# Kernel tuning notes

Hardware: AMD Instinct MI355X
Metric: run time of the kernel (lower is better)

The kernel has to match this reference:

```python
import math
import jax, jax.numpy as jnp
import numpy as np

SQRT_2_OVER_PI = 0.7978845608028654
FACIL_RATE = 2.0
FIRE_THRESH = 0.88
EPS = 1e-05

def _gelu(x):
    return 0.5 * x * (1.0 + jnp.tanh(SQRT_2_OVER_PI * (x + 0.044715 * x ** 3)))

def setup_inputs() -> dict:
    key = jax.random.key(0)
    ks = jax.random.split(key, 8)
    B, T, D, N = 4, 4096, 1024, 512
    x = jax.random.normal(ks[0], (B, T, D), jnp.float32)
    ema_x = jax.random.normal(ks[1], (D,), jnp.float32) * 0.1
    ema_x2 = ema_x ** 2 + jax.random.uniform(ks[2], (D,), jnp.float32) + 0.5
    ema_y = jax.random.normal(ks[3], (D,), jnp.float32) * 0.1
    ema_y2 = ema_y ** 2 + jax.random.uniform(ks[4], (D,), jnp.float32) + 0.5
    buf = jax.random.normal(ks[5], (N, D), jnp.float32)
    buf = buf / jnp.linalg.norm(buf, axis=-1, keepdims=True)
    facil = 1.0 + 2.0 * jax.random.uniform(ks[6], (N,), jnp.float32)  # facilitation levels >= 1
    mask = jnp.ones((N,), dtype=bool)
    return {
        'x': x,
        'log_tau_in': jnp.float32(math.log(1.0)),
        'log_tau_out': jnp.float32(math.log(1.0)),
        'log_a_in': jnp.float32(0.0),
        'log_a_out': jnp.float32(0.0),
        'log_k_boost': jnp.float32(math.log(0.5)),
        'log_k_damp': jnp.float32(math.log(0.3)),
        'ema_x': ema_x, 'ema_x2': ema_x2, 'ema_y': ema_y, 'ema_y2': ema_y2,
        'buf': buf, 'facil': facil, 'mask': mask,
    }

def reference(x, log_tau_in, log_tau_out, log_a_in, log_a_out,
              log_k_boost, log_k_damp, ema_x, ema_x2, ema_y, ema_y2,
              buf, facil, mask):
    sg = jax.lax.stop_gradient
    D = x.shape[-1]
    y = _gelu(x)
    # --- gate_211 (l1_ready steady state); z-statistics are detached in torch ---
    tau_in, tau_out = jnp.exp(log_tau_in), jnp.exp(log_tau_out)
    a_in, a_out = jax.nn.sigmoid(log_a_in), jax.nn.sigmoid(log_a_out)
    std_x = jnp.sqrt(jnp.clip(sg(ema_x2) - sg(ema_x) ** 2, 0.0)) + EPS
    z_in = jnp.mean(((sg(x) - sg(ema_x)) / std_x) ** 2, axis=-1)        # [B,T]
    std_y = jnp.sqrt(jnp.clip(sg(ema_y2) - sg(ema_y) ** 2, 0.0)) + EPS
    z_out = jnp.mean(((sg(y) - sg(ema_y)) / std_y) ** 2, axis=-1)       # [B,T]
    g_in = 1.0 - a_in + a_in * jnp.exp(-tau_in * z_in)
    g_out = 1.0 - a_out + a_out * jnp.exp(-tau_out * z_out)
    gate = g_in * g_out
    y1 = y * gate[..., None]
    # --- eval-time OCS nearest-neighbor facilitation (l2_ready, pass1_complete) ---
    k_boost = jnp.clip(jnp.exp(log_k_boost), 0.01, 4.0)
    k_damp = jnp.clip(jnp.exp(log_k_damp), 0.01, 0.9)
    y1_mean = jnp.mean(sg(y1).reshape(-1, D), axis=0)                    # [D]
    m_n = y1_mean / jnp.maximum(jnp.linalg.norm(y1_mean), 1e-12)
    buf_sg = sg(buf)
    buf_n = buf_sg / jnp.maximum(jnp.linalg.norm(buf_sg, axis=-1, keepdims=True), 1e-12)
    sims = jnp.where(mask, buf_n @ m_n, -1.0)                            # [N]
    nearest_idx = jnp.argmax(sims)
    sim_val = jnp.clip(sims[nearest_idx], 0.0, 1.0)
    fired = sim_val > FIRE_THRESH
    facil_level = sg(facil)[nearest_idx] * jnp.where(fired, FACIL_RATE, 1.0)
    v = buf_sg[nearest_idx]                                              # [D]
    valid = jnp.all(jnp.isfinite(v)) & (jnp.linalg.norm(v) >= 1e-06)
    mod = (facil_level - 1.0) * sim_val
    boost = 1.0 + sg(k_boost) * mod            # torch uses .item(): detached
    damp = jnp.maximum(0.01, 1.0 - sg(k_damp) * mod)
    proj = jnp.sum(y1 * v, axis=-1, keepdims=True)
    y_par = proj * v
    out = jnp.where(valid, y_par * boost + (y1 - y_par) * damp, y1)
    return out
```

## Files before the change

kernel.cpp:

```cpp
#include <hip/hip_runtime.h>
#include <math.h>

#define D 1024
#define NROWS 16384
#define NBUF 512
#define NBLK_A 512

#define OFF_INVSTDX 0
#define OFF_INVSTDY 1024
#define OFF_CONST   2048
#define OFF_KEY     2056
#define OFF_RES     2058
#define OFF_GATE    2064
#define OFF_MEAN    18448
#define OFF_PART    19472

__device__ __forceinline__ float4 ld4(const float* p) { return *(const float4*)p; }

__device__ __forceinline__ float wave_red(float v) {
    #pragma unroll
    for (int off = 32; off > 0; off >>= 1) v += __shfl_xor(v, off, 64);
    return v;
}

__device__ __forceinline__ float gelu_f(float x) {
    float u = 0.7978845608028654f * (x + 0.044715f * x * x * x);
    float e = __expf(2.0f * u);
    float t = 1.0f - 2.0f / (e + 1.0f);
    return 0.5f * x * (1.0f + t);
}

__global__ void k_init(const float* __restrict__ ema_x, const float* __restrict__ ema_x2,
                       const float* __restrict__ ema_y, const float* __restrict__ ema_y2,
                       const float* __restrict__ lti, const float* __restrict__ lto,
                       const float* __restrict__ lai, const float* __restrict__ lao,
                       float* __restrict__ ws) {
    int t = threadIdx.x;
    if (t < D) {
        float vx = ema_x2[t] - ema_x[t] * ema_x[t]; vx = vx > 0.f ? vx : 0.f;
        ws[OFF_INVSTDX + t] = 1.0f / (sqrtf(vx) + 1e-5f);
        float vy = ema_y2[t] - ema_y[t] * ema_y[t]; vy = vy > 0.f ? vy : 0.f;
        ws[OFF_INVSTDY + t] = 1.0f / (sqrtf(vy) + 1e-5f);
    }
    if (t == 0) {
        ws[OFF_CONST + 0] = expf(lti[0]);
        ws[OFF_CONST + 1] = expf(lto[0]);
        ws[OFF_CONST + 2] = 1.0f / (1.0f + expf(-lai[0]));
        ws[OFF_CONST + 3] = 1.0f / (1.0f + expf(-lao[0]));
        *(unsigned long long*)&ws[OFF_KEY] = 0ull;
    }
}

__global__ __launch_bounds__(256) void k_passA(const float* __restrict__ x,
                                               const float* __restrict__ ema_x,
                                               const float* __restrict__ ema_y,
                                               float* __restrict__ ws) {
    __shared__ float s_acc[D];
    const int tid = threadIdx.x;
    const int wave = tid >> 6, lane = tid & 63;
    for (int i = tid; i < D; i += 256) s_acc[i] = 0.0f;
    __syncthreads();

    const float tau_in = ws[OFF_CONST + 0], tau_out = ws[OFF_CONST + 1];
    const float a_in  = ws[OFF_CONST + 2], a_out  = ws[OFF_CONST + 3];

    int col[4];
    float4 emx[4], isx[4], emy[4], isy[4];
    #pragma unroll
    for (int j = 0; j < 4; ++j) {
        col[j] = 4 * lane + 256 * j;
        emx[j] = ld4(&ema_x[col[j]]);
        isx[j] = ld4(&ws[OFF_INVSTDX + col[j]]);
        emy[j] = ld4(&ema_y[col[j]]);
        isy[j] = ld4(&ws[OFF_INVSTDY + col[j]]);
    }
    float4 acc[4];
    #pragma unroll
    for (int j = 0; j < 4; ++j) acc[j] = make_float4(0.f, 0.f, 0.f, 0.f);

    const int gw = blockIdx.x * 4 + wave;
    const int r0 = gw * 8;
    for (int r = r0; r < r0 + 8; ++r) {
        const float* xr = x + (size_t)r * D;
        float4 yv[4];
        float zin = 0.f, zout = 0.f;
        #pragma unroll
        for (int j = 0; j < 4; ++j) {
            float4 xv = ld4(&xr[col[j]]);
            float dx, dy;
            dx = (xv.x - emx[j].x) * isx[j].x; zin += dx * dx;
            dx = (xv.y - emx[j].y) * isx[j].y; zin += dx * dx;
            dx = (xv.z - emx[j].z) * isx[j].z; zin += dx * dx;
            dx = (xv.w - emx[j].w) * isx[j].w; zin += dx * dx;
            yv[j].x = gelu_f(xv.x); dy = (yv[j].x - emy[j].x) * isy[j].x; zout += dy * dy;
            yv[j].y = gelu_f(xv.y); dy = (yv[j].y - emy[j].y) * isy[j].y; zout += dy * dy;
            yv[j].z = gelu_f(xv.z); dy = (yv[j].z - emy[j].z) * isy[j].z; zout += dy * dy;
            yv[j].w = gelu_f(xv.w); dy = (yv[j].w - emy[j].w) * isy[j].w; zout += dy * dy;
        }
        zin  = wave_red(zin)  * (1.0f / D);
        zout = wave_red(zout) * (1.0f / D);
        float g = ((1.0f - a_in)  + a_in  * __expf(-tau_in  * zin)) *
                  ((1.0f - a_out) + a_out * __expf(-tau_out * zout));
        if (lane == 0) ws[OFF_GATE + r] = g;
        #pragma unroll
        for (int j = 0; j < 4; ++j) {
            acc[j].x += yv[j].x * g;
            acc[j].y += yv[j].y * g;
            acc[j].z += yv[j].z * g;
            acc[j].w += yv[j].w * g;
        }
    }
    #pragma unroll
    for (int j = 0; j < 4; ++j) {
        atomicAdd(&s_acc[col[j] + 0], acc[j].x);
        atomicAdd(&s_acc[col[j] + 1], acc[j].y);
        atomicAdd(&s_acc[col[j] + 2], acc[j].z);
        atomicAdd(&s_acc[col[j] + 3], acc[j].w);
    }
    __syncthreads();
    float4 pv = *(float4*)&s_acc[tid * 4];
    *(float4*)&ws[OFF_PART + (size_t)blockIdx.x * D + tid * 4] = pv;
}

__global__ void k_mean(float* __restrict__ ws) {
    int d = blockIdx.x * 128 + threadIdx.x;
    float s = 0.f;
    const float* p = &ws[OFF_PART];
    for (int b = 0; b < NBLK_A; ++b) s += p[(size_t)b * D + d];
    ws[OFF_MEAN + d] = s * (1.0f / (float)NROWS);
}

__global__ __launch_bounds__(256) void k_sims(const float* __restrict__ buf,
                                              const unsigned char* __restrict__ mask,
                                              float* __restrict__ ws) {
    __shared__ float s_red[4];
    __shared__ float s_inv;
    const int tid = threadIdx.x, wave = tid >> 6, lane = tid & 63;

    float4 mv = ld4(&ws[OFF_MEAN + tid * 4]);
    float ns = mv.x * mv.x + mv.y * mv.y + mv.z * mv.z + mv.w * mv.w;
    ns = wave_red(ns);
    if (lane == 0) s_red[wave] = ns;
    __syncthreads();
    if (tid == 0) {
        float t = s_red[0] + s_red[1] + s_red[2] + s_red[3];
        s_inv = 1.0f / fmaxf(sqrtf(t), 1e-12f);
    }
    __syncthreads();
    const float inv = s_inv;

    int col[4];
    float4 mvv[4];
    #pragma unroll
    for (int j = 0; j < 4; ++j) {
        col[j] = 4 * lane + 256 * j;
        mvv[j] = ld4(&ws[OFF_MEAN + col[j]]);
    }
    unsigned long long* keyp = (unsigned long long*)&ws[OFF_KEY];
    const int gw = blockIdx.x * 4 + wave;
    for (int n = gw * 8; n < gw * 8 + 8; ++n) {
        const float* br = buf + (size_t)n * D;
        float dot = 0.f, bns = 0.f;
        #pragma unroll
        for (int j = 0; j < 4; ++j) {
            float4 bv = ld4(&br[col[j]]);
            dot += bv.x * mvv[j].x + bv.y * mvv[j].y + bv.z * mvv[j].z + bv.w * mvv[j].w;
            bns += bv.x * bv.x + bv.y * bv.y + bv.z * bv.z + bv.w * bv.w;
        }
        dot = wave_red(dot);
        bns = wave_red(bns);
        if (lane == 0) {
            float sim = -1.0f;
            if (mask[n]) sim = (dot * inv) / fmaxf(sqrtf(bns), 1e-12f);
            unsigned int fb = __float_as_uint(sim);
            unsigned int mono = (fb & 0x80000000u) ? ~fb : (fb | 0x80000000u);
            unsigned long long key = ((unsigned long long)mono << 32) | (unsigned int)(~n);
            atomicMax(keyp, key);
        }
    }
}

__global__ __launch_bounds__(1024) void k_final(const float* __restrict__ buf,
                                                const float* __restrict__ facil,
                                                const float* __restrict__ lkb,
                                                const float* __restrict__ lkd,
                                                float* __restrict__ ws) {
    __shared__ float s_sum[16];
    __shared__ int s_fin;
    const int tid = threadIdx.x, wave = tid >> 6, lane = tid & 63;
    if (tid == 0) s_fin = 1;
    __syncthreads();

    unsigned long long key = *(const unsigned long long*)&ws[OFF_KEY];
    int idx = (int)(~(unsigned int)(key & 0xFFFFFFFFull));
    unsigned int mono = (unsigned int)(key >> 32);
    unsigned int fb = (mono & 0x80000000u) ? (mono ^ 0x80000000u) : ~mono;
    float sim = __uint_as_float(fb);

    float v = buf[(size_t)idx * D + tid];
    if (!isfinite(v)) atomicAnd(&s_fin, 0);
    float ns = wave_red(v * v);
    if (lane == 0) s_sum[wave] = ns;
    __syncthreads();
    if (tid == 0) {
        float t = 0.f;
        #pragma unroll
        for (int i = 0; i < 16; ++i) t += s_sum[i];
        float nrm = sqrtf(t);
        int valid = s_fin && (nrm >= 1e-6f);
        float sim_val = fminf(fmaxf(sim, 0.0f), 1.0f);
        float fl = facil[idx] * ((sim_val > 0.88f) ? 2.0f : 1.0f);
        float mod = (fl - 1.0f) * sim_val;
        float kb = fminf(fmaxf(expf(lkb[0]), 0.01f), 4.0f);
        float kd = fminf(fmaxf(expf(lkd[0]), 0.01f), 0.9f);
        float boost = 1.0f + kb * mod;
        float damp = fmaxf(0.01f, 1.0f - kd * mod);
        int* wi = (int*)ws;
        wi[OFF_RES + 0] = idx;
        wi[OFF_RES + 1] = valid;
        ws[OFF_RES + 2] = boost;
        ws[OFF_RES + 3] = damp;
    }
}

__global__ __launch_bounds__(256) void k_passB(const float* __restrict__ x,
                                               const float* __restrict__ buf,
                                               const float* __restrict__ ws,
                                               float* __restrict__ out) {
    const int tid = threadIdx.x, wave = tid >> 6, lane = tid & 63;
    const int* wi = (const int*)ws;
    const int idx = wi[OFF_RES + 0];
    const int valid = wi[OFF_RES + 1];
    const float boost = ws[OFF_RES + 2], damp = ws[OFF_RES + 3];
    const float dampe = valid ? damp : 1.0f;
    const float coef = valid ? (boost - damp) : 0.0f;

    int col[4];
    float4 vv[4];
    const float* vrow = buf + (size_t)idx * D;
    #pragma unroll
    for (int j = 0; j < 4; ++j) {
        col[j] = 4 * lane + 256 * j;
        vv[j] = ld4(&vrow[col[j]]);
        if (!valid) vv[j] = make_float4(0.f, 0.f, 0.f, 0.f);
    }

    const int gw = blockIdx.x * 4 + wave;
    const int r0 = gw * 8;
    for (int r = r0; r < r0 + 8; ++r) {
        const float* xr = x + (size_t)r * D;
        const float g = ws[OFF_GATE + r];
        float4 y1[4];
        float proj = 0.f;
        #pragma unroll
        for (int j = 0; j < 4; ++j) {
            float4 xv = ld4(&xr[col[j]]);
            y1[j].x = gelu_f(xv.x) * g; proj += y1[j].x * vv[j].x;
            y1[j].y = gelu_f(xv.y) * g; proj += y1[j].y * vv[j].y;
            y1[j].z = gelu_f(xv.z) * g; proj += y1[j].z * vv[j].z;
            y1[j].w = gelu_f(xv.w) * g; proj += y1[j].w * vv[j].w;
        }
        proj = wave_red(proj);
        const float pc = proj * coef;
        float* orow = out + (size_t)r * D;
        #pragma unroll
        for (int j = 0; j < 4; ++j) {
            float4 o;
            o.x = y1[j].x * dampe + pc * vv[j].x;
            o.y = y1[j].y * dampe + pc * vv[j].y;
            o.z = y1[j].z * dampe + pc * vv[j].z;
            o.w = y1[j].w * dampe + pc * vv[j].w;
            *(float4*)&orow[col[j]] = o;
        }
    }
}

extern "C" void kernel_launch(void* const* d_in, const int* in_sizes, int n_in,
                              void* d_out, int out_size, void* d_ws, size_t ws_size,
                              hipStream_t stream) {
    const float* x      = (const float*)d_in[0];
    const float* lti    = (const float*)d_in[1];
    const float* lto    = (const float*)d_in[2];
    const float* lai    = (const float*)d_in[3];
    const float* lao    = (const float*)d_in[4];
    const float* lkb    = (const float*)d_in[5];
    const float* lkd    = (const float*)d_in[6];
    const float* ema_x  = (const float*)d_in[7];
    const float* ema_x2 = (const float*)d_in[8];
    const float* ema_y  = (const float*)d_in[9];
    const float* ema_y2 = (const float*)d_in[10];
    const float* buf    = (const float*)d_in[11];
    const float* facil  = (const float*)d_in[12];
    const unsigned char* mask = (const unsigned char*)d_in[13];
    float* ws  = (float*)d_ws;
    float* out = (float*)d_out;

    hipLaunchKernelGGL(k_init,  dim3(1),   dim3(1024), 0, stream,
                       ema_x, ema_x2, ema_y, ema_y2, lti, lto, lai, lao, ws);
    hipLaunchKernelGGL(k_passA, dim3(NBLK_A), dim3(256), 0, stream, x, ema_x, ema_y, ws);
    hipLaunchKernelGGL(k_mean,  dim3(8),   dim3(128),  0, stream, ws);
    hipLaunchKernelGGL(k_sims,  dim3(16),  dim3(256),  0, stream, buf, mask, ws);
    hipLaunchKernelGGL(k_final, dim3(1),   dim3(1024), 0, stream, buf, facil, lkb, lkd, ws);
    hipLaunchKernelGGL(k_passB, dim3(NBLK_A), dim3(256), 0, stream, x, buf, ws, out);
}
```

Before: 213.3 us.

## Fold init and mean kernels into passA, double grid, use nontemporal stores

Removes the separate init and mean-reduction kernels. passA now computes the inverse stds and gate constants inline and adds its per-block column sums directly into the global mean with atomics; a memset clears the workspace first. passA, sims and passB launch twice as many blocks, each handling half as many rows, with occupancy hints. The output is written with nontemporal stores. The mean is left as an unnormalized sum, which is fine because it is only used as a normalized direction, but the global float atomics add contention and make the summation order nondeterministic.

```diff
diff --git a/kernel.cpp b/kernel.cpp
--- a/kernel.cpp
+++ b/kernel.cpp
@@ -4,18 +4,20 @@
 #define D 1024
 #define NROWS 16384
 #define NBUF 512
-#define NBLK_A 512
-
-#define OFF_INVSTDX 0
-#define OFF_INVSTDY 1024
-#define OFF_CONST   2048
-#define OFF_KEY     2056
-#define OFF_RES     2058
-#define OFF_GATE    2064
-#define OFF_MEAN    18448
-#define OFF_PART    19472
+
+#define OFF_MEAN 0
+#define OFF_KEY  1024
+#define OFF_RES  1026
+#define OFF_GATE 1032
+#define ZERO_BYTES 4112
+
+typedef float nfloat4 __attribute__((ext_vector_type(4)));
 
 __device__ __forceinline__ float4 ld4(const float* p) { return *(const float4*)p; }
+__device__ __forceinline__ void st4_nt(float* p, float4 v) {
+    nfloat4 nv = { v.x, v.y, v.z, v.w };
+    __builtin_nontemporal_store(nv, (nfloat4*)p);
+}
 
 __device__ __forceinline__ float wave_red(float v) {
     #pragma unroll
@@ -30,39 +32,34 @@
     return 0.5f * x * (1.0f + t);
 }
 
-__global__ void k_init(const float* __restrict__ ema_x, const float* __restrict__ ema_x2,
-                       const float* __restrict__ ema_y, const float* __restrict__ ema_y2,
-                       const float* __restrict__ lti, const float* __restrict__ lto,
-                       const float* __restrict__ lai, const float* __restrict__ lao,
-                       float* __restrict__ ws) {
-    int t = threadIdx.x;
-    if (t < D) {
-        float vx = ema_x2[t] - ema_x[t] * ema_x[t]; vx = vx > 0.f ? vx : 0.f;
-        ws[OFF_INVSTDX + t] = 1.0f / (sqrtf(vx) + 1e-5f);
-        float vy = ema_y2[t] - ema_y[t] * ema_y[t]; vy = vy > 0.f ? vy : 0.f;
-        ws[OFF_INVSTDY + t] = 1.0f / (sqrtf(vy) + 1e-5f);
-    }
-    if (t == 0) {
-        ws[OFF_CONST + 0] = expf(lti[0]);
-        ws[OFF_CONST + 1] = expf(lto[0]);
-        ws[OFF_CONST + 2] = 1.0f / (1.0f + expf(-lai[0]));
-        ws[OFF_CONST + 3] = 1.0f / (1.0f + expf(-lao[0]));
-        *(unsigned long long*)&ws[OFF_KEY] = 0ull;
-    }
-}
-
-__global__ __launch_bounds__(256) void k_passA(const float* __restrict__ x,
-                                               const float* __restrict__ ema_x,
-                                               const float* __restrict__ ema_y,
-                                               float* __restrict__ ws) {
+__device__ __forceinline__ float4 inv_std4(float4 m, float4 m2) {
+    float4 r;
+    r.x = 1.0f / (sqrtf(fmaxf(m2.x - m.x * m.x, 0.f)) + 1e-5f);
+    r.y = 1.0f / (sqrtf(fmaxf(m2.y - m.y * m.y, 0.f)) + 1e-5f);
+    r.z = 1.0f / (sqrtf(fmaxf(m2.z - m.z * m.z, 0.f)) + 1e-5f);
+    r.w = 1.0f / (sqrtf(fmaxf(m2.w - m.w * m.w, 0.f)) + 1e-5f);
+    return r;
+}
+
+__global__ __launch_bounds__(256, 4) void k_passA(const float* __restrict__ x,
+                                                  const float* __restrict__ ema_x,
+                                                  const float* __restrict__ ema_x2,
+                                                  const float* __restrict__ ema_y,
+                                                  const float* __restrict__ ema_y2,
+                                                  const float* __restrict__ lti,
+                                                  const float* __restrict__ lto,
+                                                  const float* __restrict__ lai,
+                                                  const float* __restrict__ lao,
+                                                  float* __restrict__ ws) {
     __shared__ float s_acc[D];
     const int tid = threadIdx.x;
     const int wave = tid >> 6, lane = tid & 63;
     for (int i = tid; i < D; i += 256) s_acc[i] = 0.0f;
     __syncthreads();
 
-    const float tau_in = ws[OFF_CONST + 0], tau_out = ws[OFF_CONST + 1];
-    const float a_in  = ws[OFF_CONST + 2], a_out  = ws[OFF_CONST + 3];
+    const float tau_in = __expf(lti[0]), tau_out = __expf(lto[0]);
+    const float a_in  = 1.0f / (1.0f + __expf(-lai[0]));
+    const float a_out = 1.0f / (1.0f + __expf(-lao[0]));
 
     int col[4];
     float4 emx[4], isx[4], emy[4], isy[4];
@@ -70,17 +67,16 @@
     for (int j = 0; j < 4; ++j) {
         col[j] = 4 * lane + 256 * j;
         emx[j] = ld4(&ema_x[col[j]]);
-        isx[j] = ld4(&ws[OFF_INVSTDX + col[j]]);
+        isx[j] = inv_std4(emx[j], ld4(&ema_x2[col[j]]));
         emy[j] = ld4(&ema_y[col[j]]);
-        isy[j] = ld4(&ws[OFF_INVSTDY + col[j]]);
+        isy[j] = inv_std4(emy[j], ld4(&ema_y2[col[j]]));
     }
     float4 acc[4];
     #pragma unroll
     for (int j = 0; j < 4; ++j) acc[j] = make_float4(0.f, 0.f, 0.f, 0.f);
 
-    const int gw = blockIdx.x * 4 + wave;
-    const int r0 = gw * 8;
-    for (int r = r0; r < r0 + 8; ++r) {
+    const int r0 = (blockIdx.x * 4 + wave) * 4;
+    for (int r = r0; r < r0 + 4; ++r) {
         const float* xr = x + (size_t)r * D;
         float4 yv[4];
         float zin = 0.f, zout = 0.f;
@@ -118,16 +114,7 @@
         atomicAdd(&s_acc[col[j] + 3], acc[j].w);
     }
     __syncthreads();
-    float4 pv = *(float4*)&s_acc[tid * 4];
-    *(float4*)&ws[OFF_PART + (size_t)blockIdx.x * D + tid * 4] = pv;
-}
-
-__global__ void k_mean(float* __restrict__ ws) {
-    int d = blockIdx.x * 128 + threadIdx.x;
-    float s = 0.f;
-    const float* p = &ws[OFF_PART];
-    for (int b = 0; b < NBLK_A; ++b) s += p[(size_t)b * D + d];
-    ws[OFF_MEAN + d] = s * (1.0f / (float)NROWS);
+    for (int i = tid; i < D; i += 256) atomicAdd(&ws[OFF_MEAN + i], s_acc[i]);
 }
 
 __global__ __launch_bounds__(256) void k_sims(const float* __restrict__ buf,
@@ -157,8 +144,8 @@
         mvv[j] = ld4(&ws[OFF_MEAN + col[j]]);
     }
     unsigned long long* keyp = (unsigned long long*)&ws[OFF_KEY];
-    const int gw = blockIdx.x * 4 + wave;
-    for (int n = gw * 8; n < gw * 8 + 8; ++n) {
+    const int n0 = (blockIdx.x * 4 + wave) * 4;
+    for (int n = n0; n < n0 + 4; ++n) {
         const float* br = buf + (size_t)n * D;
         float dot = 0.f, bns = 0.f;
         #pragma unroll
@@ -223,10 +210,10 @@
     }
 }
 
-__global__ __launch_bounds__(256) void k_passB(const float* __restrict__ x,
-                                               const float* __restrict__ buf,
-                                               const float* __restrict__ ws,
-                                               float* __restrict__ out) {
+__global__ __launch_bounds__(256, 4) void k_passB(const float* __restrict__ x,
+                                                  const float* __restrict__ buf,
+                                                  const float* __restrict__ ws,
+                                                  float* __restrict__ out) {
     const int tid = threadIdx.x, wave = tid >> 6, lane = tid & 63;
     const int* wi = (const int*)ws;
     const int idx = wi[OFF_RES + 0];
@@ -245,9 +232,8 @@
         if (!valid) vv[j] = make_float4(0.f, 0.f, 0.f, 0.f);
     }
 
-    const int gw = blockIdx.x * 4 + wave;
-    const int r0 = gw * 8;
-    for (int r = r0; r < r0 + 8; ++r) {
+    const int r0 = (blockIdx.x * 4 + wave) * 4;
+    for (int r = r0; r < r0 + 4; ++r) {
         const float* xr = x + (size_t)r * D;
         const float g = ws[OFF_GATE + r];
         float4 y1[4];
@@ -270,7 +256,7 @@
             o.y = y1[j].y * dampe + pc * vv[j].y;
             o.z = y1[j].z * dampe + pc * vv[j].z;
             o.w = y1[j].w * dampe + pc * vv[j].w;
-            *(float4*)&orow[col[j]] = o;
+            st4_nt(&orow[col[j]], o);
         }
     }
 }
@@ -295,11 +281,10 @@
     float* ws  = (float*)d_ws;
     float* out = (float*)d_out;
 
-    hipLaunchKernelGGL(k_init,  dim3(1),   dim3(1024), 0, stream,
-                       ema_x, ema_x2, ema_y, ema_y2, lti, lto, lai, lao, ws);
-    hipLaunchKernelGGL(k_passA, dim3(NBLK_A), dim3(256), 0, stream, x, ema_x, ema_y, ws);
-    hipLaunchKernelGGL(k_mean,  dim3(8),   dim3(128),  0, stream, ws);
-    hipLaunchKernelGGL(k_sims,  dim3(16),  dim3(256),  0, stream, buf, mask, ws);
+    (void)hipMemsetAsync(d_ws, 0, ZERO_BYTES, stream);
+    hipLaunchKernelGGL(k_passA, dim3(1024), dim3(256), 0, stream,
+                       x, ema_x, ema_x2, ema_y, ema_y2, lti, lto, lai, lao, ws);
+    hipLaunchKernelGGL(k_sims,  dim3(32),  dim3(256), 0, stream, buf, mask, ws);
     hipLaunchKernelGGL(k_final, dim3(1),   dim3(1024), 0, stream, buf, facil, lkb, lkd, ws);
-    hipLaunchKernelGGL(k_passB, dim3(NBLK_A), dim3(256), 0, stream, x, buf, ws, out);
-}
+    hipLaunchKernelGGL(k_passB, dim3(1024), dim3(256), 0, stream, x, buf, ws, out);
+}
```

Result: faster. 196.6 us (-7.9%).
